# Performance work log

Hardware: AMD Instinct MI355X
Metric: run time of the kernel (lower is better)

## Reference

```python
import jax, jax.numpy as jnp
import numpy as np

D_MODEL = 1024
N_HEADS = 16
D_K = D_MODEL // N_HEADS
LORA_R = 8
SCALING = 16 / 8  # lora_alpha / lora_rank = 2.0


def setup_inputs() -> dict:
    key = jax.random.key(0)
    ks = jax.random.split(key, 12)
    s = 1.0 / np.sqrt(D_MODEL)
    inp = {
        "x": jax.random.normal(ks[0], (4, 2048, D_MODEL), dtype=jnp.float32),
        "w_q": jax.random.normal(ks[1], (D_MODEL, D_MODEL), dtype=jnp.float32) * s,
        "b_q": jnp.zeros((D_MODEL,), dtype=jnp.float32),
        "w_k": jax.random.normal(ks[2], (D_MODEL, D_MODEL), dtype=jnp.float32) * s,
        "b_k": jnp.zeros((D_MODEL,), dtype=jnp.float32),
        "w_v": jax.random.normal(ks[3], (D_MODEL, D_MODEL), dtype=jnp.float32) * s,
        "b_v": jnp.zeros((D_MODEL,), dtype=jnp.float32),
        "w_o": jax.random.normal(ks[4], (D_MODEL, D_MODEL), dtype=jnp.float32) * s,
        "b_o": jnp.zeros((D_MODEL,), dtype=jnp.float32),
        # LoRA: down [d_model -> r], up [r -> d_model]; up init nonzero here so grads flow
        "a_q": jax.random.normal(ks[5], (D_MODEL, LORA_R), dtype=jnp.float32) * s,
        "u_q": jax.random.normal(ks[6], (LORA_R, D_MODEL), dtype=jnp.float32) * 0.01,
        "a_k": jax.random.normal(ks[7], (D_MODEL, LORA_R), dtype=jnp.float32) * s,
        "u_k": jax.random.normal(ks[8], (LORA_R, D_MODEL), dtype=jnp.float32) * 0.01,
        "a_v": jax.random.normal(ks[9], (D_MODEL, LORA_R), dtype=jnp.float32) * s,
        "u_v": jax.random.normal(ks[10], (LORA_R, D_MODEL), dtype=jnp.float32) * 0.01,
    }
    return inp


def reference(x, w_q, b_q, w_k, b_k, w_v, b_v, w_o, b_o, a_q, u_q, a_k, u_k, a_v, u_v):
    B, S, D = x.shape
    # base projections + LoRA (eval mode: dropout off)
    q = x @ w_q + b_q + (x @ a_q) @ u_q * SCALING
    k = x @ w_k + b_k + (x @ a_k) @ u_k * SCALING
    v = x @ w_v + b_v + (x @ a_v) @ u_v * SCALING
    # [B, H, S, d_k]
    q = q.reshape(B, S, N_HEADS, D_K).transpose(0, 2, 1, 3)
    k = k.reshape(B, S, N_HEADS, D_K).transpose(0, 2, 1, 3)
    v = v.reshape(B, S, N_HEADS, D_K).transpose(0, 2, 1, 3)
    scores = jnp.einsum("bhsd,bhtd->bhst", q, k) / np.sqrt(D_K)
    probs = jax.nn.softmax(scores, axis=-1)
    out = jnp.einsum("bhst,bhtd->bhsd", probs, v)
    out = out.transpose(0, 2, 1, 3).reshape(B, S, D)
    return out @ w_o + b_o
```

## Files before the change

kernel.cpp:

```cpp
#include <hip/hip_runtime.h>
#include <stdint.h>

typedef unsigned short u16;
typedef unsigned int u32;
typedef __bf16 bf16x8 __attribute__((ext_vector_type(8)));
typedef __bf16 bf16x4 __attribute__((ext_vector_type(4)));
typedef float f32x4 __attribute__((ext_vector_type(4)));
typedef float f32x16 __attribute__((ext_vector_type(16)));
typedef u32 u32x4 __attribute__((ext_vector_type(4)));

#define SEQ 2048
#define QSCALE 0.1803368801111137f

__device__ __forceinline__ float fast_exp2(float x) { return __builtin_amdgcn_exp2f(x); }

__device__ __forceinline__ void async16(const void* g, void* l) {
  __builtin_amdgcn_global_load_lds((const __attribute__((address_space(1))) void*)g,
                                   (__attribute__((address_space(3))) void*)l, 16, 0, 0);
}

__device__ __forceinline__ u32 pkbf(float a, float b) {
  u16 xa = __builtin_bit_cast(u16, (__bf16)a);
  u16 xb = __builtin_bit_cast(u16, (__bf16)b);
  return (u32)xa | ((u32)xb << 16);
}


__global__ void prep_all_kernel(const float* __restrict__ x, u16* __restrict__ xb,
                                const float* __restrict__ wq, const float* __restrict__ wk,
                                const float* __restrict__ wv, const float* __restrict__ wo,
                                const float* __restrict__ aq, const float* __restrict__ ak,
                                const float* __restrict__ av,
                                const float* __restrict__ uq, const float* __restrict__ uk,
                                const float* __restrict__ uv,
                                u16* __restrict__ weffT,
                                const float* __restrict__ bq, const float* __restrict__ bk,
                                const float* __restrict__ bv, float* __restrict__ bias_qkv) {
  __shared__ float wt[32][33];
  __shared__ float at[32][8];
  __shared__ float ut[8][33];
  const int bid = blockIdx.x;
  const int t = threadIdx.x;
  if (bid < 8192) {
    int i = (bid * 256 + t) * 4;
    float4 v = *(const float4*)(x + i);
    bf16x4 o;
    o[0] = (__bf16)v.x; o[1] = (__bf16)v.y; o[2] = (__bf16)v.z; o[3] = (__bf16)v.w;
    *(bf16x4*)(xb + i) = o;
  } else if (bid < 12288) {
    const int p = (bid - 8192) >> 10, bx = (bid - 8192) & 1023;
    const int tn0 = (bx & 31) * 32, tk0 = (bx >> 5) * 32;
    const float* w = (p == 0) ? wq : (p == 1) ? wk : (p == 2) ? wv : wo;
    const float* a = (p == 0) ? aq : (p == 1) ? ak : av;
    const float* u = (p == 0) ? uq : (p == 1) ? uk : uv;
    {
      int tk = t >> 3, tn4 = (t & 7) * 4;
      float4 v = *(const float4*)(w + (tk0 + tk) * 1024 + tn0 + tn4);
      wt[tk][tn4] = v.x; wt[tk][tn4 + 1] = v.y; wt[tk][tn4 + 2] = v.z; wt[tk][tn4 + 3] = v.w;
    }
    if (p < 3) {
      at[t >> 3][t & 7] = a[(tk0 + (t >> 3)) * 8 + (t & 7)];
      ut[t >> 5][t & 31] = u[(t >> 5) * 1024 + tn0 + (t & 31)];
    }
    __syncthreads();
    const int tn = t >> 3, tk4 = (t & 7) * 4;
    bf16x4 o;
#pragma unroll
    for (int jj = 0; jj < 4; ++jj) {
      int k = tk4 + jj;
      float val = wt[k][tn];
      if (p < 3) {
        float acc = 0.f;
#pragma unroll
        for (int r = 0; r < 8; ++r) acc += at[k][r] * ut[r][tn];
        val += 2.0f * acc;
      }
      if (p == 0) val *= QSCALE;
      o[jj] = (__bf16)val;
    }
    *(bf16x4*)(weffT + p * 1048576 + (tn0 + tn) * 1024 + tk0 + tk4) = o;
  } else {
    int i = (bid - 12288) * 256 + t;
    bias_qkv[i] = (i < 1024) ? bq[i] * QSCALE : (i < 2048) ? bk[i - 1024] : bv[i - 2048];
  }
}


template <int MODE>
__global__ __launch_bounds__(256, 2)
void gemm_tt(const u16* __restrict__ U, const u16* __restrict__ V, void* __restrict__ OUT,
             u16* __restrict__ vT, const float* __restrict__ bias, const int NU, const int K) {
  __shared__ __align__(16) char smU[8192];
  __shared__ __align__(16) char smV[8192];
  const int t = threadIdx.x;
  const int lane = t & 63, ln = lane & 15, g = lane >> 4, w = t >> 6;
  const int u0 = blockIdx.x * 128, v0 = blockIdx.y * 128;
  const int wu = (w & 1) * 64, wv = (w >> 1) * 64;
  f32x4 acc[4][4] = {};
  for (int k0 = 0; k0 < K; k0 += 32) {
    __syncthreads();
#pragma unroll
    for (int half = 0; half < 2; ++half) {
      int p = half * 256 + t;
      int s = p >> 2, cp = p & 3;
      int c = cp ^ (s & 3);
      int ldsoff = (half * 256 + (t & 192)) * 16;
      async16(U + (u0 + s) * K + k0 + c * 8, smU + ldsoff);
      async16(V + (v0 + s) * K + k0 + c * 8, smV + ldsoff);
    }
    __syncthreads();
    bf16x8 af[4], bf[4];
#pragma unroll
    for (int mt = 0; mt < 4; ++mt)
      af[mt] = *(const bf16x8*)(smU + (wu + mt * 16 + ln) * 64 + ((g ^ (ln & 3)) * 16));
#pragma unroll
    for (int nt = 0; nt < 4; ++nt)
      bf[nt] = *(const bf16x8*)(smV + (wv + nt * 16 + ln) * 64 + ((g ^ (ln & 3)) * 16));
#pragma unroll
    for (int mt = 0; mt < 4; ++mt)
#pragma unroll
      for (int nt = 0; nt < 4; ++nt)
        acc[mt][nt] = __builtin_amdgcn_mfma_f32_16x16x32_bf16(af[mt], bf[nt], acc[mt][nt], 0, 0, 0);
  }
  const bool isV = (MODE == 1) && (u0 + wu >= 2048);
#pragma unroll
  for (int mt = 0; mt < 4; ++mt) {
    const int u = u0 + wu + mt * 16 + g * 4;
    const float4 bs = *(const float4*)(bias + u);
#pragma unroll
    for (int nt = 0; nt < 4; ++nt) {
      const int v = v0 + wv + nt * 16 + ln;
      f32x4 a = acc[mt][nt];
      a[0] += bs.x; a[1] += bs.y; a[2] += bs.z; a[3] += bs.w;
      if (MODE == 0) {
        *(float4*)((float*)OUT + (size_t)v * NU + u) = make_float4(a[0], a[1], a[2], a[3]);
      } else if (!isV) {
        bf16x4 o;
        o[0] = (__bf16)a[0]; o[1] = (__bf16)a[1]; o[2] = (__bf16)a[2]; o[3] = (__bf16)a[3];
        *(bf16x4*)((u16*)OUT + (size_t)v * 2048 + u) = o;
      } else {
        const int uu = u - 2048;
        const int hh = uu >> 6, dd = uu & 63;
        const int bb = v >> 11, ss = v & 2047;
        u16* dst = vT + ((size_t)((bb * 16 + hh) * 64 + dd)) * 2048 + ss;
#pragma unroll
        for (int r = 0; r < 4; ++r)
          *(__bf16*)(dst + (size_t)r * 2048) = (__bf16)a[r];
      }
    }
  }
}


__global__ __launch_bounds__(256, 3)
void attn_kernel(const u16* __restrict__ qkv, const u16* __restrict__ vT,
                 u16* __restrict__ attn_o) {
  __shared__ __align__(16) char smK[16384];
  __shared__ __align__(16) char smVt[16384];
  const int t = threadIdx.x;
  const int lane = t & 63, q32 = lane & 31, hf = lane >> 5, w = t >> 6;
  const int hd = blockIdx.x, qt = blockIdx.y, b = blockIdx.z;
  const int q0 = qt * 128;
  const size_t base_b = (size_t)b * SEQ * 2048;
  const u16* qbase = qkv + base_b + hd * 64;
  const u16* kbase0 = qkv + base_b + 1024 + hd * 64;
  const u16* vbase0 = vT + ((size_t)(b * 16 + hd) * 64) * 2048;

  bf16x8 qf[4];
#pragma unroll
  for (int ks = 0; ks < 4; ++ks)
    qf[ks] = *(const bf16x8*)(qbase + (size_t)(q0 + w * 32 + q32) * 2048 + ks * 16 + hf * 8);

  const u16* srcK[4];
  const u16* srcV[4];
  char* dstK[4];
  char* dstV[4];
#pragma unroll
  for (int i = 0; i < 4; ++i) {
    int p = i * 256 + t;
    {
      int row = p >> 3, cp = p & 7, c = cp ^ (row & 7);
      srcK[i] = kbase0 + (size_t)row * 2048 + c * 8;
      dstK[i] = smK + (i * 256 + (t & 192)) * 16;
    }
    {
      int d = p >> 4, cp = p & 15;
      int key = (d & 15) ^ (d >> 3);
      int c = (cp ^ key) & 15;
      srcV[i] = vbase0 + (size_t)d * 2048 + c * 8;
      dstV[i] = smVt + (i * 256 + (t & 192)) * 16;
    }
  }

  f32x16 accO[2] = {};
  float l_acc = 0.f;

  for (int kt = 0; kt < 16; ++kt) {
    __syncthreads();
#pragma unroll
    for (int i = 0; i < 4; ++i) {
      async16(srcK[i], dstK[i]);
      srcK[i] += 128 * 2048;
    }
#pragma unroll
    for (int i = 0; i < 4; ++i) {
      async16(srcV[i], dstV[i]);
      srcV[i] += 128;
    }
    __syncthreads();

    f32x16 st[4] = {};
#pragma unroll
    for (int ks = 0; ks < 4; ++ks) {
#pragma unroll
      for (int c = 0; c < 4; ++c) {
        int row = c * 32 + q32;
        bf16x8 kfr = *(const bf16x8*)(smK + row * 128 + (((2 * ks + hf) ^ (row & 7)) * 16));
        st[c] = __builtin_amdgcn_mfma_f32_32x32x16_bf16(kfr, qf[ks], st[c], 0, 0, 0);
      }
    }

#pragma unroll
    for (int c = 0; c < 4; ++c) {
      float e[16];
#pragma unroll
      for (int r = 0; r < 16; ++r) {
        e[r] = fast_exp2(st[c][r]);
        l_acc += e[r];
      }
#pragma unroll
      for (int kh = 0; kh < 2; ++kh) {
        u32 A0 = pkbf(e[8 * kh + 0], e[8 * kh + 1]);
        u32 A1 = pkbf(e[8 * kh + 2], e[8 * kh + 3]);
        u32 A2 = pkbf(e[8 * kh + 4], e[8 * kh + 5]);
        u32 A3 = pkbf(e[8 * kh + 6], e[8 * kh + 7]);
        u32 t0 = hf ? A0 : A2;
        u32 t1 = hf ? A1 : A3;
        u32 P0 = (u32)__shfl_xor((int)t0, 32);
        u32 P1 = (u32)__shfl_xor((int)t1, 32);
        u32x4 bw;
        bw[0] = hf ? P0 : A0;
        bw[1] = hf ? P1 : A1;
        bw[2] = hf ? A2 : P0;
        bw[3] = hf ? A3 : P1;
        bf16x8 pfrag = __builtin_bit_cast(bf16x8, bw);
#pragma unroll
        for (int mt = 0; mt < 2; ++mt) {
          int row = mt * 32 + q32;
          int key = (row & 15) ^ (row >> 3);
          bf16x8 vfr = *(const bf16x8*)(smVt + row * 256 +
                                        (((4 * c + 2 * kh + hf) ^ key) & 15) * 16);
          accO[mt] = __builtin_amdgcn_mfma_f32_32x32x16_bf16(vfr, pfrag, accO[mt], 0, 0, 0);
        }
      }
    }
  }

  float l_tot = l_acc + __shfl_xor(l_acc, 32);
  float il = 1.0f / l_tot;
  const int s = q0 + w * 32 + q32;
#pragma unroll
  for (int mt = 0; mt < 2; ++mt)
#pragma unroll
    for (int qd = 0; qd < 4; ++qd) {
      int d0 = 32 * mt + 8 * qd + 4 * hf;
      bf16x4 o;
#pragma unroll
      for (int r = 0; r < 4; ++r) o[r] = (__bf16)(accO[mt][4 * qd + r] * il);
      *(bf16x4*)(attn_o + (size_t)(b * SEQ + s) * 1024 + hd * 64 + d0) = o;
    }
}


extern "C" void kernel_launch(void* const* d_in, const int* in_sizes, int n_in,
                              void* d_out, int out_size, void* d_ws, size_t ws_size,
                              hipStream_t stream) {
  const float* x  = (const float*)d_in[0];
  const float* wq = (const float*)d_in[1];
  const float* bq = (const float*)d_in[2];
  const float* wk = (const float*)d_in[3];
  const float* bk = (const float*)d_in[4];
  const float* wv = (const float*)d_in[5];
  const float* bv = (const float*)d_in[6];
  const float* wo = (const float*)d_in[7];
  const float* bo = (const float*)d_in[8];
  const float* aq = (const float*)d_in[9];
  const float* uq = (const float*)d_in[10];
  const float* ak = (const float*)d_in[11];
  const float* uk = (const float*)d_in[12];
  const float* av = (const float*)d_in[13];
  const float* uv = (const float*)d_in[14];

  char* ws = (char*)d_ws;
  u16* xb       = (u16*)(ws);
  u16* attn_o   = (u16*)(ws);
  u16* qkv      = (u16*)(ws + (16u << 20));
  u16* vT       = (u16*)(ws + (48u << 20));
  u16* weffT    = (u16*)(ws + (64u << 20));
  float* biasq  = (float*)(ws + (72u << 20));

  prep_all_kernel<<<dim3(12300), dim3(256), 0, stream>>>(
      x, xb, wq, wk, wv, wo, aq, ak, av, uq, uk, uv, weffT, bq, bk, bv, biasq);
  gemm_tt<1><<<dim3(24, 64), dim3(256), 0, stream>>>(weffT, xb, (void*)qkv, vT, biasq, 2048, 1024);
  attn_kernel<<<dim3(16, 16, 4), dim3(256), 0, stream>>>(qkv, vT, attn_o);
  gemm_tt<0><<<dim3(8, 64), dim3(256), 0, stream>>>(weffT + 3u * 1048576u, attn_o, d_out, nullptr, bo, 1024, 1024);
}
```

Baseline: 313.1 us.

## Permute K rows to drop P-fragment shuffles and sum softmax denominator via MFMA

Loads K tiles with a row permutation so the score MFMA output layout already matches the B-operand layout of the PV MFMA, removing the cross-half lane shuffles and selects used to build P fragments. The per-row softmax denominator is no longer summed with scalar adds; an extra MFMA against a ones fragment (nonzero only in lane 0) accumulates the row sums, which are then broadcast with one shuffle at the end. The aim is to cut VALU and cross-lane work in the inner loop, at the cost of one extra MFMA per P fragment and a full extra accumulator register set.

```diff
diff --git a/kernel.cpp b/kernel.cpp
--- a/kernel.cpp
+++ b/kernel.cpp
@@ -171,6 +171,13 @@
   for (int ks = 0; ks < 4; ++ks)
     qf[ks] = *(const bf16x8*)(qbase + (size_t)(q0 + w * 32 + q32) * 2048 + ks * 16 + hf * 8);
 
+  bf16x8 ones_frag;
+  {
+    u32 o2 = (q32 == 0) ? 0x3F803F80u : 0u;
+    u32x4 ow = {o2, o2, o2, o2};
+    ones_frag = __builtin_bit_cast(bf16x8, ow);
+  }
+
   const u16* srcK[4];
   const u16* srcV[4];
   char* dstK[4];
@@ -179,8 +186,10 @@
   for (int i = 0; i < 4; ++i) {
     int p = i * 256 + t;
     {
-      int row = p >> 3, cp = p & 7, c = cp ^ (row & 7);
-      srcK[i] = kbase0 + (size_t)row * 2048 + c * 8;
+      int row = p >> 3, cp = p & 7;
+      int rowp = (row & ~12) | ((row & 4) << 1) | ((row & 8) >> 1);
+      int c = cp ^ (row & 7);
+      srcK[i] = kbase0 + (size_t)rowp * 2048 + c * 8;
       dstK[i] = smK + (i * 256 + (t & 192)) * 16;
     }
     {
@@ -193,7 +202,7 @@
   }
 
   f32x16 accO[2] = {};
-  float l_acc = 0.f;
+  f32x16 acc_l = {};
 
   for (int kt = 0; kt < 16; ++kt) {
     __syncthreads();
@@ -222,28 +231,18 @@
 
 #pragma unroll
     for (int c = 0; c < 4; ++c) {
-      float e[16];
-#pragma unroll
-      for (int r = 0; r < 16; ++r) {
-        e[r] = fast_exp2(st[c][r]);
-        l_acc += e[r];
-      }
 #pragma unroll
       for (int kh = 0; kh < 2; ++kh) {
-        u32 A0 = pkbf(e[8 * kh + 0], e[8 * kh + 1]);
-        u32 A1 = pkbf(e[8 * kh + 2], e[8 * kh + 3]);
-        u32 A2 = pkbf(e[8 * kh + 4], e[8 * kh + 5]);
-        u32 A3 = pkbf(e[8 * kh + 6], e[8 * kh + 7]);
-        u32 t0 = hf ? A0 : A2;
-        u32 t1 = hf ? A1 : A3;
-        u32 P0 = (u32)__shfl_xor((int)t0, 32);
-        u32 P1 = (u32)__shfl_xor((int)t1, 32);
+        float e[8];
+#pragma unroll
+        for (int j = 0; j < 8; ++j) e[j] = fast_exp2(st[c][8 * kh + j]);
         u32x4 bw;
-        bw[0] = hf ? P0 : A0;
-        bw[1] = hf ? P1 : A1;
-        bw[2] = hf ? A2 : P0;
-        bw[3] = hf ? A3 : P1;
+        bw[0] = pkbf(e[0], e[1]);
+        bw[1] = pkbf(e[2], e[3]);
+        bw[2] = pkbf(e[4], e[5]);
+        bw[3] = pkbf(e[6], e[7]);
         bf16x8 pfrag = __builtin_bit_cast(bf16x8, bw);
+        acc_l = __builtin_amdgcn_mfma_f32_32x32x16_bf16(ones_frag, pfrag, acc_l, 0, 0, 0);
 #pragma unroll
         for (int mt = 0; mt < 2; ++mt) {
           int row = mt * 32 + q32;
@@ -256,8 +255,8 @@
     }
   }
 
-  float l_tot = l_acc + __shfl_xor(l_acc, 32);
-  float il = 1.0f / l_tot;
+  float lv = __shfl(acc_l[0], q32);
+  float il = 1.0f / lv;
   const int s = q0 + w * 32 + q32;
 #pragma unroll
   for (int mt = 0; mt < 2; ++mt)
```

Measured after the change: 314.6 us. About the same (+0.5%).
